# Kernel tuning notes

Hardware: AMD Instinct MI355X
Metric: run time of the kernel (lower is better)

The kernel has to match this reference:

```python
import jax, jax.numpy as jnp
import numpy as np

N, L, H, D = 2, 4096, 12, 64
HD = H * D

def setup_inputs() -> dict:
    key = jax.random.key(0)
    ks = jax.random.split(key, 5)
    s = 1.0 / np.sqrt(HD)  # keep projections well-scaled
    return {
        "x": jax.random.normal(ks[0], (N, L, HD), dtype=jnp.float32),
        "Wq": jax.random.normal(ks[1], (HD, HD), dtype=jnp.float32) * s,
        "bq": jnp.zeros((HD,), dtype=jnp.float32),
        "Wk": jax.random.normal(ks[2], (HD, HD), dtype=jnp.float32) * s,
        "bk": jnp.zeros((HD,), dtype=jnp.float32),
        "Wv": jax.random.normal(ks[3], (HD, HD), dtype=jnp.float32) * s,
        "bv": jnp.zeros((HD,), dtype=jnp.float32),
        "Wo": jax.random.normal(ks[4], (HD, HD), dtype=jnp.float32) * s,
        "bo": jnp.zeros((HD,), dtype=jnp.float32),
        "train": 0,
    }

def reference(x, Wq, bq, Wk, bk, Wv, bv, Wo, bo, train):
    n, l, hd = x.shape
    h, d = H, D
    # QKV projections (hk.Linear: x @ W + b), reshape to (n, l, h, d)
    q = (x @ Wq + bq).reshape(n, l, h, d)
    k = (x @ Wk + bk).reshape(n, l, h, d)
    v = (x @ Wv + bv).reshape(n, l, h, d)
    # scores: (n, q, k, h), scaled by sqrt(key_size)
    qkt = jnp.einsum('nqhd,nkhd->nqkh', q, k) / jnp.sqrt(jnp.float32(d))
    attn = jax.nn.softmax(qkt, axis=2)
    # eval mode: dropout_rate is 0.0, so dropout is identity
    o = jnp.einsum('nqkh,nkhd->nqhd', attn, v).reshape(n, l, hd)
    return o @ Wo + bo
```

## Files before the change

kernel.cpp:

```cpp
#include <hip/hip_runtime.h>

#define NN 2
#define LL 4096
#define HH 12
#define DD 64
#define HD_ 768
#define M_TOT (NN * LL)

typedef __bf16 bf16_t;
typedef __bf16 bf16x8 __attribute__((ext_vector_type(8)));
typedef float floatx4 __attribute__((ext_vector_type(4)));

#define QSCALE 0.1803368801111f

__device__ __forceinline__ void async_load16(const bf16_t* g, bf16_t* l) {
    __builtin_amdgcn_global_load_lds(
        (const __attribute__((address_space(1))) unsigned int*)(g),
        (__attribute__((address_space(3))) unsigned int*)(l),
        16, 0, 0);
}

__global__ void cvt_kernel(const float* __restrict__ src, bf16_t* __restrict__ dst, int n4) {
    int i = blockIdx.x * blockDim.x + threadIdx.x;
    if (i < n4) {
        const float4 v = ((const float4*)src)[i];
        bf16_t* d = dst + (size_t)i * 4;
        d[0] = (bf16_t)v.x; d[1] = (bf16_t)v.y; d[2] = (bf16_t)v.z; d[3] = (bf16_t)v.w;
    }
}

__global__ void cvt_wt_kernel(const float* __restrict__ W, bf16_t* __restrict__ Wt) {
    int id = blockIdx.x * 256 + threadIdx.x;
    int k = id / HD_;
    int n = id % HD_;
    Wt[(size_t)n * HD_ + k] = (bf16_t)W[id];
}

__global__ __launch_bounds__(256) void gemm_kernel(
    const bf16_t* __restrict__ A, const bf16_t* __restrict__ Bt,
    const float* __restrict__ bias, void* __restrict__ Cout, int mode, float scale)
{
    __shared__ __align__(16) bf16_t As[64 * 72];
    __shared__ __align__(16) bf16_t Bs[64 * 72];

    const int tid  = threadIdx.x;
    const int wave = tid >> 6, lane = tid & 63;
    const int quad = lane >> 4, l16 = lane & 15;
    const int wm = wave >> 1, wn = wave & 1;
    const int m0 = blockIdx.y * 64, n0 = blockIdx.x * 64;

    const int lrow = tid >> 2;
    const int lcol = (tid & 3) * 16;

    floatx4 acc[2][2] = {};

    for (int kt = 0; kt < HD_; kt += 64) {
        __syncthreads();
        {
            const bf16_t* ga = A + (size_t)(m0 + lrow) * HD_ + kt + lcol;
            *(bf16x8*)&As[lrow * 72 + lcol]     = *(const bf16x8*)ga;
            *(bf16x8*)&As[lrow * 72 + lcol + 8] = *(const bf16x8*)(ga + 8);
            const bf16_t* gb = Bt + (size_t)(n0 + lrow) * HD_ + kt + lcol;
            *(bf16x8*)&Bs[lrow * 72 + lcol]     = *(const bf16x8*)gb;
            *(bf16x8*)&Bs[lrow * 72 + lcol + 8] = *(const bf16x8*)(gb + 8);
        }
        __syncthreads();
        for (int ks = 0; ks < 2; ++ks) {
            bf16x8 af[2], bfr[2];
            af[0]  = *(const bf16x8*)&As[(wm * 32 + l16) * 72 + ks * 32 + quad * 8];
            af[1]  = *(const bf16x8*)&As[(wm * 32 + 16 + l16) * 72 + ks * 32 + quad * 8];
            bfr[0] = *(const bf16x8*)&Bs[(wn * 32 + l16) * 72 + ks * 32 + quad * 8];
            bfr[1] = *(const bf16x8*)&Bs[(wn * 32 + 16 + l16) * 72 + ks * 32 + quad * 8];
            for (int mi = 0; mi < 2; ++mi)
                for (int ni = 0; ni < 2; ++ni)
                    acc[mi][ni] = __builtin_amdgcn_mfma_f32_16x16x32_bf16(
                        af[mi], bfr[ni], acc[mi][ni], 0, 0, 0);
        }
    }

    for (int ni = 0; ni < 2; ++ni) {
        const int col = n0 + wn * 32 + ni * 16 + l16;
        const float bv = bias[col];
        for (int mi = 0; mi < 2; ++mi) {
            for (int r = 0; r < 4; ++r) {
                const int row = m0 + wm * 32 + mi * 16 + quad * 4 + r;
                const float val = (acc[mi][ni][r] + bv) * scale;
                if (mode == 3) {
                    ((float*)Cout)[(size_t)row * HD_ + col] = val;
                } else {
                    const int nn = row >> 12, l = row & 4095;
                    const int h = col >> 6, d = col & 63;
                    bf16_t* o = (bf16_t*)Cout;
                    if (mode == 2)
                        o[(((size_t)nn * HH + h) * DD + d) * LL + l] = (bf16_t)val;
                    else
                        o[(((size_t)nn * HH + h) * LL + l) * DD + d] = (bf16_t)val;
                }
            }
        }
    }
}

__global__ __launch_bounds__(256) void attn_kernel(
    const bf16_t* __restrict__ qg, const bf16_t* __restrict__ kg,
    const bf16_t* __restrict__ vtg, bf16_t* __restrict__ og)
{
    __shared__ __align__(16) bf16_t Ks[8 * 64 * 8];
    __shared__ __align__(16) bf16_t Vs[8 * 64 * 8];
    __shared__ __align__(16) bf16_t Ps[4][4 * 64 * 8];

    const int tid  = threadIdx.x;
    const int w    = tid >> 6, lane = tid & 63;
    const int quad = lane >> 4, l16 = lane & 15;
    const int qt0  = blockIdx.x * 128;
    const int nh   = blockIdx.y;
    const int nIdx = nh / HH, hIdx = nh % HH;
    const size_t headL = (size_t)nh * LL;

    bf16x8 aq[2][2];
    for (int mi = 0; mi < 2; ++mi) {
        const int row = qt0 + w * 32 + mi * 16 + l16;
        const bf16_t* qp = qg + (headL + row) * DD + quad * 8;
        aq[mi][0] = *(const bf16x8*)qp;
        aq[mi][1] = *(const bf16x8*)(qp + 32);
    }

    const bf16_t* kptr = kg + (headL + w * 16 + l16) * DD + quad * 8;
    const bf16_t* vptr = vtg + ((size_t)nh * DD + w * 16 + l16) * LL + quad * 8;
    bf16_t* ldsK0 = &Ks[(0 * 4 + w) * 512];
    bf16_t* ldsK1 = &Ks[(1 * 4 + w) * 512];
    bf16_t* ldsV0 = &Vs[(0 * 4 + w) * 512];
    bf16_t* ldsV1 = &Vs[(1 * 4 + w) * 512];

    int pb[4];
    for (int nf = 0; nf < 4; ++nf) {
        const int kv = nf * 16 + l16;
        pb[nf] = (kv >> 5) * 512 + ((kv >> 3) & 3) * 128 + (kv & 7) + quad * 32;
    }
    bf16_t* PsW = Ps[w];

    floatx4 oacc[2][4] = {};
    float rowsum[2][4] = {};

    for (int t = 0; t < LL / 64; ++t) {
        __syncthreads();
        async_load16(kptr,      ldsK0);
        async_load16(kptr + 32, ldsK1);
        async_load16(vptr,      ldsV0);
        async_load16(vptr + 32, ldsV1);
        kptr += 64 * DD;
        vptr += 64;
        __syncthreads();

        floatx4 sacc[2][4] = {};
        for (int ks = 0; ks < 2; ++ks) {
            for (int nf = 0; nf < 4; ++nf) {
                bf16x8 bk = *(const bf16x8*)&Ks[(ks * 4 + nf) * 512 + lane * 8];
                sacc[0][nf] = __builtin_amdgcn_mfma_f32_16x16x32_bf16(aq[0][ks], bk, sacc[0][nf], 0, 0, 0);
                sacc[1][nf] = __builtin_amdgcn_mfma_f32_16x16x32_bf16(aq[1][ks], bk, sacc[1][nf], 0, 0, 0);
            }
        }

        for (int mi = 0; mi < 2; ++mi) {
            bf16_t* pw = PsW + mi * 1024;
            for (int nf = 0; nf < 4; ++nf) {
                for (int r = 0; r < 4; ++r) {
                    const float p = __builtin_amdgcn_exp2f(sacc[mi][nf][r]);
                    rowsum[mi][r] += p;
                    pw[pb[nf] + r * 8] = (bf16_t)p;
                }
            }
        }

        for (int ks2 = 0; ks2 < 2; ++ks2) {
            bf16x8 ap0 = *(const bf16x8*)&PsW[(0 * 2 + ks2) * 512 + lane * 8];
            bf16x8 ap1 = *(const bf16x8*)&PsW[(1 * 2 + ks2) * 512 + lane * 8];
            for (int df = 0; df < 4; ++df) {
                bf16x8 bv = *(const bf16x8*)&Vs[(ks2 * 4 + df) * 512 + lane * 8];
                oacc[0][df] = __builtin_amdgcn_mfma_f32_16x16x32_bf16(ap0, bv, oacc[0][df], 0, 0, 0);
                oacc[1][df] = __builtin_amdgcn_mfma_f32_16x16x32_bf16(ap1, bv, oacc[1][df], 0, 0, 0);
            }
        }
    }

    for (int mi = 0; mi < 2; ++mi)
        for (int r = 0; r < 4; ++r) {
            float s = rowsum[mi][r];
            s += __shfl_xor(s, 1);
            s += __shfl_xor(s, 2);
            s += __shfl_xor(s, 4);
            s += __shfl_xor(s, 8);
            rowsum[mi][r] = __builtin_amdgcn_rcpf(s);
        }

    for (int mi = 0; mi < 2; ++mi) {
        for (int df = 0; df < 4; ++df) {
            const int col = hIdx * 64 + df * 16 + l16;
            for (int r = 0; r < 4; ++r) {
                const int row = qt0 + w * 32 + mi * 16 + quad * 4 + r;
                og[((size_t)nIdx * LL + row) * HD_ + col] =
                    (bf16_t)(oacc[mi][df][r] * rowsum[mi][r]);
            }
        }
    }
}

extern "C" void kernel_launch(void* const* d_in, const int* in_sizes, int n_in,
                              void* d_out, int out_size, void* d_ws, size_t ws_size,
                              hipStream_t stream) {
    const float* x  = (const float*)d_in[0];
    const float* Wq = (const float*)d_in[1];
    const float* bq = (const float*)d_in[2];
    const float* Wk = (const float*)d_in[3];
    const float* bk = (const float*)d_in[4];
    const float* Wv = (const float*)d_in[5];
    const float* bv = (const float*)d_in[6];
    const float* Wo = (const float*)d_in[7];
    const float* bo = (const float*)d_in[8];

    char* ws = (char*)d_ws;
    const size_t xbytes = (size_t)M_TOT * HD_ * 2;
    const size_t wbytes = (size_t)HD_ * HD_ * 2;

    bf16_t* xb  = (bf16_t*)ws; ws += xbytes;
    bf16_t* wqt = (bf16_t*)ws; ws += wbytes;
    bf16_t* wkt = (bf16_t*)ws; ws += wbytes;
    bf16_t* wvt = (bf16_t*)ws; ws += wbytes;
    bf16_t* wot = (bf16_t*)ws; ws += wbytes;
    bf16_t* qb  = (bf16_t*)ws; ws += xbytes;
    bf16_t* kb  = (bf16_t*)ws; ws += xbytes;
    bf16_t* vtb = (bf16_t*)ws; ws += xbytes;
    bf16_t* ob  = (bf16_t*)ws; ws += xbytes;

    cvt_kernel<<<(M_TOT * HD_ / 4 + 255) / 256, 256, 0, stream>>>(x, xb, M_TOT * HD_ / 4);
    cvt_wt_kernel<<<HD_ * HD_ / 256, 256, 0, stream>>>(Wq, wqt);
    cvt_wt_kernel<<<HD_ * HD_ / 256, 256, 0, stream>>>(Wk, wkt);
    cvt_wt_kernel<<<HD_ * HD_ / 256, 256, 0, stream>>>(Wv, wvt);
    cvt_wt_kernel<<<HD_ * HD_ / 256, 256, 0, stream>>>(Wo, wot);

    dim3 gg(HD_ / 64, M_TOT / 64);
    gemm_kernel<<<gg, 256, 0, stream>>>(xb, wqt, bq, (void*)qb, 0, QSCALE);
    gemm_kernel<<<gg, 256, 0, stream>>>(xb, wkt, bk, (void*)kb, 1, 1.0f);
    gemm_kernel<<<gg, 256, 0, stream>>>(xb, wvt, bv, (void*)vtb, 2, 1.0f);

    attn_kernel<<<dim3(LL / 128, NN * HH), 256, 0, stream>>>(qb, kb, vtb, ob);

    gemm_kernel<<<gg, 256, 0, stream>>>(ob, wot, bo, d_out, 3, 1.0f);
}
```

Baseline: 360.5 us.

## Batch QKV and weight-convert launches, keep attention probabilities in registers

```diff
diff --git a/kernel.cpp b/kernel.cpp
--- a/kernel.cpp
+++ b/kernel.cpp
@@ -8,7 +8,12 @@
 #define M_TOT (NN * LL)
 
 typedef __bf16 bf16_t;
+typedef _Float16 f16_t;
 typedef __bf16 bf16x8 __attribute__((ext_vector_type(8)));
+typedef __bf16 bf16x4 __attribute__((ext_vector_type(4)));
+typedef _Float16 f16x2 __attribute__((ext_vector_type(2)));
+typedef _Float16 f16x4 __attribute__((ext_vector_type(4)));
+typedef _Float16 f16x8 __attribute__((ext_vector_type(8)));
 typedef float floatx4 __attribute__((ext_vector_type(4)));
 
 #define QSCALE 0.1803368801111f
@@ -18,6 +23,10 @@
         (const __attribute__((address_space(1))) unsigned int*)(g),
         (__attribute__((address_space(3))) unsigned int*)(l),
         16, 0, 0);
+}
+
+__device__ __forceinline__ f16x2 pkrtz(float a, float b) {
+    return __builtin_bit_cast(f16x2, __builtin_amdgcn_cvt_pkrtz(a, b));
 }
 
 __global__ void cvt_kernel(const float* __restrict__ src, bf16_t* __restrict__ dst, int n4) {
@@ -29,30 +38,26 @@
     }
 }
 
-__global__ void cvt_wt_kernel(const float* __restrict__ W, bf16_t* __restrict__ Wt) {
+struct WtArgs { const float* W[4]; bf16_t* Wt[4]; };
+__global__ void cvt_wt_kernel(WtArgs a) {
+    const int z = blockIdx.z;
     int id = blockIdx.x * 256 + threadIdx.x;
     int k = id / HD_;
     int n = id % HD_;
-    Wt[(size_t)n * HD_ + k] = (bf16_t)W[id];
-}
-
-__global__ __launch_bounds__(256) void gemm_kernel(
+    a.Wt[z][(size_t)n * HD_ + k] = (bf16_t)a.W[z][id];
+}
+
+__device__ __forceinline__ void gemm_tile64(
     const bf16_t* __restrict__ A, const bf16_t* __restrict__ Bt,
-    const float* __restrict__ bias, void* __restrict__ Cout, int mode, float scale)
+    bf16_t* As, bf16_t* Bs, int m0, int n0, floatx4 (&acc)[2][2])
 {
-    __shared__ __align__(16) bf16_t As[64 * 72];
-    __shared__ __align__(16) bf16_t Bs[64 * 72];
-
     const int tid  = threadIdx.x;
-    const int wave = tid >> 6, lane = tid & 63;
+    const int lane = tid & 63;
     const int quad = lane >> 4, l16 = lane & 15;
+    const int wave = tid >> 6;
     const int wm = wave >> 1, wn = wave & 1;
-    const int m0 = blockIdx.y * 64, n0 = blockIdx.x * 64;
-
     const int lrow = tid >> 2;
     const int lcol = (tid & 3) * 16;
-
-    floatx4 acc[2][2] = {};
 
     for (int kt = 0; kt < HD_; kt += 64) {
         __syncthreads();
@@ -77,37 +82,88 @@
                         af[mi], bfr[ni], acc[mi][ni], 0, 0, 0);
         }
     }
+}
+
+struct QKVArgs {
+    const bf16_t* Bt[3];
+    const float* bias[3];
+    void* out[3];
+};
+__global__ __launch_bounds__(256) void gemm_qkv_kernel(const bf16_t* __restrict__ A, QKVArgs p)
+{
+    __shared__ __align__(16) bf16_t As[64 * 72];
+    __shared__ __align__(16) bf16_t Bs[64 * 72];
+    const int z = blockIdx.z;
+    const int m0 = blockIdx.y * 64, n0 = blockIdx.x * 64;
+
+    floatx4 acc[2][2] = {};
+    gemm_tile64(A, p.Bt[z], As, Bs, m0, n0, acc);
+
+    const int tid  = threadIdx.x;
+    const int lane = tid & 63;
+    const int quad = lane >> 4, l16 = lane & 15;
+    const int wave = tid >> 6;
+    const int wm = wave >> 1, wn = wave & 1;
+    const float scale = (z == 0) ? QSCALE : 1.0f;
+    const float* bias = p.bias[z];
 
     for (int ni = 0; ni < 2; ++ni) {
         const int col = n0 + wn * 32 + ni * 16 + l16;
         const float bv = bias[col];
+        const int h = col >> 6, d = col & 63;
         for (int mi = 0; mi < 2; ++mi) {
             for (int r = 0; r < 4; ++r) {
                 const int row = m0 + wm * 32 + mi * 16 + quad * 4 + r;
                 const float val = (acc[mi][ni][r] + bv) * scale;
-                if (mode == 3) {
-                    ((float*)Cout)[(size_t)row * HD_ + col] = val;
-                } else {
-                    const int nn = row >> 12, l = row & 4095;
-                    const int h = col >> 6, d = col & 63;
-                    bf16_t* o = (bf16_t*)Cout;
-                    if (mode == 2)
-                        o[(((size_t)nn * HH + h) * DD + d) * LL + l] = (bf16_t)val;
-                    else
-                        o[(((size_t)nn * HH + h) * LL + l) * DD + d] = (bf16_t)val;
-                }
+                const int nn = row >> 12, l = row & 4095;
+                if (z == 2)
+                    ((f16_t*)p.out[2])[(((size_t)nn * HH + h) * DD + d) * LL + l] = (f16_t)val;
+                else
+                    ((bf16_t*)p.out[z])[(((size_t)nn * HH + h) * LL + l) * DD + d] = (bf16_t)val;
             }
         }
+    }
+}
+
+__global__ __launch_bounds__(256) void gemm_o_kernel(
+    const bf16_t* __restrict__ A, const bf16_t* __restrict__ Bt,
+    const float* __restrict__ bias, float* __restrict__ Cout)
+{
+    __shared__ __align__(16) bf16_t As[64 * 72];
+    __shared__ __align__(16) bf16_t Bs[64 * 72];
+    const int m0 = blockIdx.y * 64, n0 = blockIdx.x * 64;
+
+    floatx4 acc[2][2] = {};
+    gemm_tile64(A, Bt, As, Bs, m0, n0, acc);
+
+    const int tid  = threadIdx.x;
+    const int lane = tid & 63;
+    const int quad = lane >> 4, l16 = lane & 15;
+    const int wave = tid >> 6;
+    const int wm = wave >> 1, wn = wave & 1;
+
+    for (int ni = 0; ni < 2; ++ni) {
+        const int col = n0 + wn * 32 + ni * 16 + l16;
+        const float bv = bias[col];
+        for (int mi = 0; mi < 2; ++mi)
+            for (int r = 0; r < 4; ++r) {
+                const int row = m0 + wm * 32 + mi * 16 + quad * 4 + r;
+                Cout[(size_t)row * HD_ + col] = acc[mi][ni][r] + bv;
+            }
     }
 }
 
 __global__ __launch_bounds__(256) void attn_kernel(
     const bf16_t* __restrict__ qg, const bf16_t* __restrict__ kg,
-    const bf16_t* __restrict__ vtg, bf16_t* __restrict__ og)
+    const f16_t* __restrict__ vtg, bf16_t* __restrict__ og)
 {
-    __shared__ __align__(16) bf16_t Ks[8 * 64 * 8];
-    __shared__ __align__(16) bf16_t Vs[8 * 64 * 8];
-    __shared__ __align__(16) bf16_t Ps[4][4 * 64 * 8];
+    __shared__ union {
+        struct {
+            bf16_t Ks[8 * 64 * 8];
+            f16_t  Va[16 * 64 * 4];
+        } s;
+        bf16_t OT[128 * 72];
+    } u;
 
     const int tid  = threadIdx.x;
     const int w    = tid >> 6, lane = tid & 63;
@@ -117,92 +173,97 @@
     const int nIdx = nh / HH, hIdx = nh % HH;
     const size_t headL = (size_t)nh * LL;
 
-    bf16x8 aq[2][2];
+    bf16x8 bq[2][2];
     for (int mi = 0; mi < 2; ++mi) {
         const int row = qt0 + w * 32 + mi * 16 + l16;
         const bf16_t* qp = qg + (headL + row) * DD + quad * 8;
-        aq[mi][0] = *(const bf16x8*)qp;
-        aq[mi][1] = *(const bf16x8*)(qp + 32);
+        bq[mi][0] = *(const bf16x8*)qp;
+        bq[mi][1] = *(const bf16x8*)(qp + 32);
     }
 
     const bf16_t* kptr = kg + (headL + w * 16 + l16) * DD + quad * 8;
-    const bf16_t* vptr = vtg + ((size_t)nh * DD + w * 16 + l16) * LL + quad * 8;
-    bf16_t* ldsK0 = &Ks[(0 * 4 + w) * 512];
-    bf16_t* ldsK1 = &Ks[(1 * 4 + w) * 512];
-    bf16_t* ldsV0 = &Vs[(0 * 4 + w) * 512];
-    bf16_t* ldsV1 = &Vs[(1 * 4 + w) * 512];
-
-    int pb[4];
-    for (int nf = 0; nf < 4; ++nf) {
-        const int kv = nf * 16 + l16;
-        pb[nf] = (kv >> 5) * 512 + ((kv >> 3) & 3) * 128 + (kv & 7) + quad * 32;
-    }
-    bf16_t* PsW = Ps[w];
-
-    floatx4 oacc[2][4] = {};
-    float rowsum[2][4] = {};
+    bf16_t* ldsK0 = &u.s.Ks[(0 * 4 + w) * 512];
+    bf16_t* ldsK1 = &u.s.Ks[(1 * 4 + w) * 512];
+
+    const int dsrc = tid >> 2, cch = tid & 3;
+    const f16_t* vptr = vtg + ((size_t)nh * DD + dsrc) * LL + cch * 16;
+    f16_t* vdst = &u.s.Va[((cch * 4 + (dsrc >> 4)) * 64 + (dsrc & 15)) * 4];
+
+    floatx4 oacc[4][2] = {};
+    float rowsum[2] = {0.f, 0.f};
 
     for (int t = 0; t < LL / 64; ++t) {
+        f16x8 v0 = *(const f16x8*)vptr;
+        f16x8 v1 = *(const f16x8*)(vptr + 8);
+        vptr += 64;
         __syncthreads();
         async_load16(kptr,      ldsK0);
         async_load16(kptr + 32, ldsK1);
-        async_load16(vptr,      ldsV0);
-        async_load16(vptr + 32, ldsV1);
         kptr += 64 * DD;
-        vptr += 64;
+        *(f16x4*)(vdst +   0) = __builtin_shufflevector(v0, v0, 0, 1, 2, 3);
+        *(f16x4*)(vdst +  64) = __builtin_shufflevector(v0, v0, 4, 5, 6, 7);
+        *(f16x4*)(vdst + 128) = __builtin_shufflevector(v1, v1, 0, 1, 2, 3);
+        *(f16x4*)(vdst + 192) = __builtin_shufflevector(v1, v1, 4, 5, 6, 7);
         __syncthreads();
 
-        floatx4 sacc[2][4] = {};
-        for (int ks = 0; ks < 2; ++ks) {
-            for (int nf = 0; nf < 4; ++nf) {
-                bf16x8 bk = *(const bf16x8*)&Ks[(ks * 4 + nf) * 512 + lane * 8];
-                sacc[0][nf] = __builtin_amdgcn_mfma_f32_16x16x32_bf16(aq[0][ks], bk, sacc[0][nf], 0, 0, 0);
-                sacc[1][nf] = __builtin_amdgcn_mfma_f32_16x16x32_bf16(aq[1][ks], bk, sacc[1][nf], 0, 0, 0);
-            }
+        floatx4 sacc[4][2] = {};
+        for (int ks = 0; ks < 2; ++ks)
+            for (int kb = 0; kb < 4; ++kb) {
+                bf16x8 ak = *(const bf16x8*)&u.s.Ks[(ks * 4 + kb) * 512 + lane * 8];
+                sacc[kb][0] = __builtin_amdgcn_mfma_f32_16x16x32_bf16(ak, bq[0][ks], sacc[kb][0], 0, 0, 0);
+                sacc[kb][1] = __builtin_amdgcn_mfma_f32_16x16x32_bf16(ak, bq[1][ks], sacc[kb][1], 0, 0, 0);
+            }
+
+        f16x4 pf[4][2];
+        for (int kb = 0; kb < 4; ++kb)
+            for (int mi = 0; mi < 2; ++mi) {
+                const float p0 = __builtin_amdgcn_exp2f(sacc[kb][mi][0]);
+                const float p1 = __builtin_amdgcn_exp2f(sacc[kb][mi][1]);
+                const float p2 = __builtin_amdgcn_exp2f(sacc[kb][mi][2]);
+                const float p3 = __builtin_amdgcn_exp2f(sacc[kb][mi][3]);
+                rowsum[mi] += (p0 + p1) + (p2 + p3);
+                f16x2 lo = pkrtz(p0, p1);
+                f16x2 hi = pkrtz(p2, p3);
+                pf[kb][mi] = __builtin_shufflevector(lo, hi, 0, 1, 2, 3);
+            }
+
+        for (int kb = 0; kb < 4; ++kb)
+            for (int db = 0; db < 4; ++db) {
+                f16x4 av = *(const f16x4*)&u.s.Va[(kb * 4 + db) * 256 + lane * 4];
+                oacc[db][0] = __builtin_amdgcn_mfma_f32_16x16x16f16(av, pf[kb][0], oacc[db][0], 0, 0, 0);
+                oacc[db][1] = __builtin_amdgcn_mfma_f32_16x16x16f16(av, pf[kb][1], oacc[db][1], 0, 0, 0);
+            }
+    }
+
+    float rinv[2];
+    for (int mi = 0; mi < 2; ++mi) {
+        float s = rowsum[mi];
+        s += __shfl_xor(s, 16);
+        s += __shfl_xor(s, 32);
+        rinv[mi] = __builtin_amdgcn_rcpf(s);
+    }
+
+    __syncthreads();
+    for (int db = 0; db < 4; ++db)
+        for (int mi = 0; mi < 2; ++mi) {
+            bf16x4 o4;
+            for (int r = 0; r < 4; ++r)
+                o4[r] = (bf16_t)(oacc[db][mi][r] * rinv[mi]);
+            *(bf16x4*)&u.OT[(w * 32 + mi * 16 + l16) * 72 + db * 16 + quad * 4] = o4;
         }
-
-        for (int mi = 0; mi < 2; ++mi) {
-            bf16_t* pw = PsW + mi * 1024;
-            for (int nf = 0; nf < 4; ++nf) {
-                for (int r = 0; r < 4; ++r) {
-                    const float p = __builtin_amdgcn_exp2f(sacc[mi][nf][r]);
-                    rowsum[mi][r] += p;
-                    pw[pb[nf] + r * 8] = (bf16_t)p;
-                }
-            }
-        }
-
-        for (int ks2 = 0; ks2 < 2; ++ks2) {
-            bf16x8 ap0 = *(const bf16x8*)&PsW[(0 * 2 + ks2) * 512 + lane * 8];
-            bf16x8 ap1 = *(const bf16x8*)&PsW[(1 * 2 + ks2) * 512 + lane * 8];
-            for (int df = 0; df < 4; ++df) {
-                bf16x8 bv = *(const bf16x8*)&Vs[(ks2 * 4 + df) * 512 + lane * 8];
-                oacc[0][df] = __builtin_amdgcn_mfma_f32_16x16x32_bf16(ap0, bv, oacc[0][df], 0, 0, 0);
-                oacc[1][df] = __builtin_amdgcn_mfma_f32_16x16x32_bf16(ap1, bv, oacc[1][df], 0, 0, 0);
-            }
-        }
-    }
-
-    for (int mi = 0; mi < 2; ++mi)
-        for (int r = 0; r < 4; ++r) {
-            float s = rowsum[mi][r];
-            s += __shfl_xor(s, 1);
-            s += __shfl_xor(s, 2);
-            s += __shfl_xor(s, 4);
-            s += __shfl_xor(s, 8);
-            rowsum[mi][r] = __builtin_amdgcn_rcpf(s);
-        }
-
-    for (int mi = 0; mi < 2; ++mi) {
-        for (int df = 0; df < 4; ++df) {
-            const int col = hIdx * 64 + df * 16 + l16;
-            for (int r = 0; r < 4; ++r) {
-                const int row = qt0 + w * 32 + mi * 16 + quad * 4 + r;
-                og[((size_t)nIdx * LL + row) * HD_ + col] =
-                    (bf16_t)(oacc[mi][df][r] * rowsum[mi][r]);
-            }
-        }
-    }
+    __syncthreads();
+
+    const int q = tid >> 1, hf = tid & 1;
+    const bf16_t* src = &u.OT[q * 72 + hf * 32];
+    bf16x8 r0 = *(const bf16x8*)(src + 0);
+    bf16x8 r1 = *(const bf16x8*)(src + 8);
+    bf16x8 r2 = *(const bf16x8*)(src + 16);
+    bf16x8 r3 = *(const bf16x8*)(src + 24);
+    bf16_t* dst = og + ((size_t)nIdx * LL + qt0 + q) * HD_ + hIdx * 64 + hf * 32;
+    *(bf16x8*)(dst + 0)  = r0;
+    *(bf16x8*)(dst + 8)  = r1;
+    *(bf16x8*)(dst + 16) = r2;
+    *(bf16x8*)(dst + 24) = r3;
 }
 
 extern "C" void kernel_launch(void* const* d_in, const int* in_sizes, int n_in,
@@ -229,21 +290,23 @@
     bf16_t* wot = (bf16_t*)ws; ws += wbytes;
     bf16_t* qb  = (bf16_t*)ws; ws += xbytes;
     bf16_t* kb  = (bf16_t*)ws; ws += xbytes;
-    bf16_t* vtb = (bf16_t*)ws; ws += xbytes;
+    f16_t*  vtb = (f16_t*)ws;  ws += xbytes;
     bf16_t* ob  = (bf16_t*)ws; ws += xbytes;
 
     cvt_kernel<<<(M_TOT * HD_ / 4 + 255) / 256, 256, 0, stream>>>(x, xb, M_TOT * HD_ / 4);
-    cvt_wt_kernel<<<HD_ * HD_ / 256, 256, 0, stream>>>(Wq, wqt);
-    cvt_wt_kernel<<<HD_ * HD_ / 256, 256, 0, stream>>>(Wk, wkt);
-    cvt_wt_kernel<<<HD_ * HD_ / 256, 256, 0, stream>>>(Wv, wvt);
-    cvt_wt_kernel<<<HD_ * HD_ / 256, 256, 0, stream>>>(Wo, wot);
-
-    dim3 gg(HD_ / 64, M_TOT / 64);
-    gemm_kernel<<<gg, 256, 0, stream>>>(xb, wqt, bq, (void*)qb, 0, QSCALE);
-    gemm_kernel<<<gg, 256, 0, stream>>>(xb, wkt, bk, (void*)kb, 1, 1.0f);
-    gemm_kernel<<<gg, 256, 0, stream>>>(xb, wvt, bv, (void*)vtb, 2, 1.0f);
+
+    WtArgs wa;
+    wa.W[0] = Wq; wa.W[1] = Wk; wa.W[2] = Wv; wa.W[3] = Wo;
+    wa.Wt[0] = wqt; wa.Wt[1] = wkt; wa.Wt[2] = wvt; wa.Wt[3] = wot;
+    cvt_wt_kernel<<<dim3(HD_ * HD_ / 256, 1, 4), 256, 0, stream>>>(wa);
+
+    QKVArgs qa;
+    qa.Bt[0] = wqt; qa.Bt[1] = wkt; qa.Bt[2] = wvt;
+    qa.bias[0] = bq; qa.bias[1] = bk; qa.bias[2] = bv;
+    qa.out[0] = qb; qa.out[1] = kb; qa.out[2] = vtb;
+    gemm_qkv_kernel<<<dim3(HD_ / 64, M_TOT / 64, 3), 256, 0, stream>>>(xb, qa);
 
     attn_kernel<<<dim3(LL / 128, NN * HH), 256, 0, stream>>>(qb, kb, vtb, ob);
 
-    gemm_kernel<<<gg, 256, 0, stream>>>(ob, wot, bo, d_out, 3, 1.0f);
-}
+    gemm_o_kernel<<<dim3(HD_ / 64, M_TOT / 64), 256, 0, stream>>>(ob, wot, bo, (float*)d_out);
+}
```

Result: no change. 366.4 us (+1.6%).
